# Kernel optimization log

Hardware: AMD Instinct MI355X
Metric: run time of the kernel (lower is better)

## Reference

```python
import jax, jax.numpy as jnp
import numpy as np

B, S, R, H = 16, 1024, 512, 512
HD = H // 2           # per-direction LSTM hidden
G = 4 * HD            # LSTM gate width
D_IN = 3 * H          # fusion encoder input size


def setup_inputs() -> dict:
    key = jax.random.key(0)
    ks = jax.random.split(key, 14)
    sc_ref = 1.0 / np.sqrt(H)
    sc_ih = 1.0 / np.sqrt(D_IN)
    sc_hh = 1.0 / np.sqrt(HD)
    return {
        "src_enc_state": jax.random.normal(ks[0], (2, B, HD), jnp.float32),  # unused by module
        "src_memory_bank": jax.random.normal(ks[1], (S, B, H), jnp.float32),
        "ref_memory_bank": jax.random.normal(ks[2], (R, B, H), jnp.float32),
        "W_ref": jax.random.normal(ks[3], (H, H), jnp.float32) * sc_ref,
        "b_ref": jax.random.normal(ks[4], (H,), jnp.float32) * sc_ref,
        "W_ih_f": jax.random.normal(ks[5], (G, D_IN), jnp.float32) * sc_ih,
        "W_hh_f": jax.random.normal(ks[6], (G, HD), jnp.float32) * sc_hh,
        "b_ih_f": jax.random.normal(ks[7], (G,), jnp.float32) * sc_hh,
        "b_hh_f": jax.random.normal(ks[8], (G,), jnp.float32) * sc_hh,
        "W_ih_b": jax.random.normal(ks[9], (G, D_IN), jnp.float32) * sc_ih,
        "W_hh_b": jax.random.normal(ks[10], (G, HD), jnp.float32) * sc_hh,
        "b_ih_b": jax.random.normal(ks[11], (G,), jnp.float32) * sc_hh,
        "b_hh_b": jax.random.normal(ks[12], (G,), jnp.float32) * sc_hh,
        "ref_length": jnp.full((B,), R, dtype=jnp.int32),  # full lengths -> pack is identity
    }


def _lstm_dir(x, W_ih, W_hh, b_ih, b_hh, reverse=False):
    """Single-direction LSTM (PyTorch gate order i,f,g,o). x: [T,B,D] -> [T,B,HD]."""
    if reverse:
        x = x[::-1]
    xg = jnp.einsum('tbd,gd->tbg', x, W_ih) + b_ih + b_hh  # precompute input gates

    def step(carry, xg_t):
        h, c = carry
        g = xg_t + h @ W_hh.T
        i, f, gg, o = jnp.split(g, 4, axis=-1)
        c = jax.nn.sigmoid(f) * c + jax.nn.sigmoid(i) * jnp.tanh(gg)
        h = jax.nn.sigmoid(o) * jnp.tanh(c)
        return (h, c), h

    h0 = jnp.zeros((x.shape[1], W_hh.shape[1]), x.dtype)
    _, hs = jax.lax.scan(step, (h0, h0), xg)
    return hs[::-1] if reverse else hs


def reference(src_enc_state, src_memory_bank, ref_memory_bank,
              W_ref, b_ref,
              W_ih_f, W_hh_f, b_ih_f, b_hh_f,
              W_ih_b, W_hh_b, b_ih_b, b_hh_b,
              ref_length):
    # --- co-attention ---
    # h_s = tanh(linear_ref(src)) : [B,S,H]
    h_s = jnp.tanh(jnp.einsum('sbh,oh->bso', src_memory_bank, W_ref) + b_ref)
    h_r = ref_memory_bank.transpose(1, 0, 2)                      # [B,R,H]
    l = jnp.einsum('bsh,brh->bsr', h_s, h_r)                      # scores [B,S,R]
    a_s = jax.nn.softmax(l, axis=1)                               # softmax over src dim
    a_r = jax.nn.softmax(l, axis=2)                               # softmax over ref dim
    c_s = jnp.einsum('brh,bsr->bhs', h_r, a_s)                    # [B,H,S]
    s_t = h_s.transpose(0, 2, 1)                                  # [B,H,S]
    cat_sc = jnp.concatenate([s_t, c_s], axis=1)                  # [B,2H,S]
    c_r = jnp.einsum('bks,bsr->brk', cat_sc, a_r)                 # [B,R,2H]
    bilstm_in = jnp.concatenate([c_r, h_r], axis=2).transpose(1, 0, 2)  # [R,B,3H]
    # --- fusion BiLSTM encoder (all lengths == R, so packing is identity) ---
    hf = _lstm_dir(bilstm_in, W_ih_f, W_hh_f, b_ih_f, b_hh_f, reverse=False)
    hb = _lstm_dir(bilstm_in, W_ih_b, W_hh_b, b_ih_b, b_hh_b, reverse=True)
    return jnp.concatenate([hf, hb], axis=-1)                     # [R,B,H]
```

## Files before the change

### kernel.cpp

```cpp
#include <hip/hip_runtime.h>
#include <hip/hip_bf16.h>
#include <math.h>

#define B_   16
#define S_   1024
#define R_   512
#define H_   512
#define HD_  256
#define G_   1024
#define DIN_ 1536

template<int EPI, int REMAP_A>
__global__ __launch_bounds__(256) void gemm_mk_nk(
    const float* __restrict__ A, long a_rs, long a_bs,
    const float* __restrict__ Bm, long b_rs, long b_bs,
    float* __restrict__ C, long c_rs, long c_bs,
    const float* __restrict__ bias,
    int M, int N, int K)
{
    __shared__ float As[16][68];
    __shared__ float Bs[16][68];
    const int bb = blockIdx.z;
    const float* Ab = A + (long)bb * a_bs;
    const float* Bb = Bm + (long)bb * b_bs;
    float* Cb = C + (long)bb * c_bs;
    const int m0 = blockIdx.y * 64, n0 = blockIdx.x * 64;
    const int tid = threadIdx.x;
    const int tx = tid & 15, ty = tid >> 4;
    const int lr = tid >> 2;
    const int lk = (tid & 3) << 2;

    long arow;
    {
        int m = m0 + lr;
        if (REMAP_A) arow = (long)((m % S_) * B_ + (m / S_)) * a_rs;
        else         arow = (long)m * a_rs;
    }
    const long brow = (long)(n0 + lr) * b_rs;

    float acc[4][4] = {};
    for (int k0 = 0; k0 < K; k0 += 16) {
        float4 av = *(const float4*)(Ab + arow + k0 + lk);
        float4 bv = *(const float4*)(Bb + brow + k0 + lk);
        As[lk + 0][lr] = av.x; As[lk + 1][lr] = av.y;
        As[lk + 2][lr] = av.z; As[lk + 3][lr] = av.w;
        Bs[lk + 0][lr] = bv.x; Bs[lk + 1][lr] = bv.y;
        Bs[lk + 2][lr] = bv.z; Bs[lk + 3][lr] = bv.w;
        __syncthreads();
#pragma unroll
        for (int kk = 0; kk < 16; ++kk) {
            float4 a = *(const float4*)&As[kk][ty << 2];
            float4 b = *(const float4*)&Bs[kk][tx << 2];
            acc[0][0] += a.x * b.x; acc[0][1] += a.x * b.y; acc[0][2] += a.x * b.z; acc[0][3] += a.x * b.w;
            acc[1][0] += a.y * b.x; acc[1][1] += a.y * b.y; acc[1][2] += a.y * b.z; acc[1][3] += a.y * b.w;
            acc[2][0] += a.z * b.x; acc[2][1] += a.z * b.y; acc[2][2] += a.z * b.z; acc[2][3] += a.z * b.w;
            acc[3][0] += a.w * b.x; acc[3][1] += a.w * b.y; acc[3][2] += a.w * b.z; acc[3][3] += a.w * b.w;
        }
        __syncthreads();
    }
#pragma unroll
    for (int i = 0; i < 4; ++i) {
        const int m = m0 + (ty << 2) + i;
#pragma unroll
        for (int j = 0; j < 4; ++j) {
            const int n = n0 + (tx << 2) + j;
            float v = acc[i][j];
            if (EPI == 1) v = tanhf(v + bias[n]);
            Cb[(long)m * c_rs + n] = v;
        }
    }
}

__device__ inline unsigned short bf16_rtn(float x)
{
    unsigned u = __float_as_uint(x);
    u += 0x7FFFu + ((u >> 16) & 1);
    return (unsigned short)(u >> 16);
}

__device__ inline unsigned pk_bf16(float lo, float hi)
{
    return (unsigned)bf16_rtn(lo) | ((unsigned)bf16_rtn(hi) << 16);
}

__global__ __launch_bounds__(256) void pack_bf16(const float* __restrict__ src,
                                                 unsigned short* __restrict__ dst,
                                                 long n4)
{
    const long i = (long)blockIdx.x * 256 + threadIdx.x;
    if (i >= n4) return;
    const float4 v = *((const float4*)src + i);
    uint2 u;
    u.x = pk_bf16(v.x, v.y);
    u.y = pk_bf16(v.z, v.w);
    *((uint2*)dst + i) = u;
}

__global__ __launch_bounds__(256) void softmax_rows(float* __restrict__ l)
{
    const int lane = threadIdx.x & 63;
    const int wv = threadIdx.x >> 6;
    const long row = (long)blockIdx.x * 4 + wv;
    float* p = l + row * R_;
    float4 v0 = ((const float4*)p)[lane * 2];
    float4 v1 = ((const float4*)p)[lane * 2 + 1];
    float m = fmaxf(fmaxf(fmaxf(v0.x, v0.y), fmaxf(v0.z, v0.w)),
                    fmaxf(fmaxf(v1.x, v1.y), fmaxf(v1.z, v1.w)));
#pragma unroll
    for (int o = 32; o; o >>= 1) m = fmaxf(m, __shfl_xor(m, o));
    v0.x = __expf(v0.x - m); v0.y = __expf(v0.y - m);
    v0.z = __expf(v0.z - m); v0.w = __expf(v0.w - m);
    v1.x = __expf(v1.x - m); v1.y = __expf(v1.y - m);
    v1.z = __expf(v1.z - m); v1.w = __expf(v1.w - m);
    float s = v0.x + v0.y + v0.z + v0.w + v1.x + v1.y + v1.z + v1.w;
#pragma unroll
    for (int o = 32; o; o >>= 1) s += __shfl_xor(s, o);
    const float inv = 1.f / s;
    v0.x *= inv; v0.y *= inv; v0.z *= inv; v0.w *= inv;
    v1.x *= inv; v1.y *= inv; v1.z *= inv; v1.w *= inv;
    ((float4*)p)[lane * 2] = v0;
    ((float4*)p)[lane * 2 + 1] = v1;
}

__global__ __launch_bounds__(512) void softmax_cols(const float* __restrict__ l,
                                                    unsigned short* __restrict__ asb)
{
    const int b = blockIdx.y;
    const int rl = threadIdx.x & 127;
    const int r = blockIdx.x * 128 + rl;
    const int sg = threadIdx.x >> 7;
    const int s0 = sg * (S_ / 4), s1 = s0 + S_ / 4;
    const float* base = l + (long)b * S_ * R_ + r;
    __shared__ float red[4][128];

    float pm = -1e30f;
    for (int s = s0; s < s1; ++s) pm = fmaxf(pm, base[(long)s * R_]);
    red[sg][rl] = pm;
    __syncthreads();
    const float m = fmaxf(fmaxf(red[0][rl], red[1][rl]), fmaxf(red[2][rl], red[3][rl]));
    __syncthreads();

    float ps = 0.f;
    for (int s = s0; s < s1; ++s) ps += __expf(base[(long)s * R_] - m);
    red[sg][rl] = ps;
    __syncthreads();
    const float inv = 1.f / (red[0][rl] + red[1][rl] + red[2][rl] + red[3][rl]);

    unsigned short* ob = asb + (long)b * S_ * R_ + r;
    for (int s = s0; s < s1; ++s)
        ob[(long)s * R_] = bf16_rtn(__expf(base[(long)s * R_] - m) * inv);
}

__global__ __launch_bounds__(256) void transpose_hs(const float* __restrict__ hs,
                                                    unsigned short* __restrict__ catb)
{
    __shared__ float tile[32][33];
    const int b = blockIdx.z;
    const int s0 = blockIdx.x * 32, h0 = blockIdx.y * 32;
    const int tx = threadIdx.x, ty = threadIdx.y;
#pragma unroll
    for (int i = 0; i < 32; i += 8)
        tile[ty + i][tx] = hs[((long)b * S_ + s0 + ty + i) * H_ + h0 + tx];
    __syncthreads();
#pragma unroll
    for (int i = 0; i < 32; i += 8)
        catb[((long)b * 2 * H_ + h0 + ty + i) * S_ + s0 + tx] = bf16_rtn(tile[tx][ty + i]);
}

__global__ __launch_bounds__(256) void transpose_ref(const float* __restrict__ ref,
                                                     unsigned short* __restrict__ refT)
{
    __shared__ float tile[32][33];
    const int b = blockIdx.z;
    const int r0 = blockIdx.x * 32, h0 = blockIdx.y * 32;
    const int tx = threadIdx.x, ty = threadIdx.y;
#pragma unroll
    for (int i = 0; i < 32; i += 8)
        tile[ty + i][tx] = ref[((long)(r0 + ty + i) * B_ + b) * H_ + h0 + tx];
    __syncthreads();
#pragma unroll
    for (int i = 0; i < 32; i += 8)
        refT[((long)b * H_ + h0 + ty + i) * R_ + r0 + tx] = bf16_rtn(tile[tx][ty + i]);
}

__global__ __launch_bounds__(256) void transpose_arT(const float* __restrict__ l,
                                                     unsigned short* __restrict__ arT)
{
    __shared__ float tile[32][33];
    const int b = blockIdx.z;
    const int s0 = blockIdx.x * 32, r0 = blockIdx.y * 32;
    const int tx = threadIdx.x, ty = threadIdx.y;
#pragma unroll
    for (int i = 0; i < 32; i += 8)
        tile[ty + i][tx] = l[((long)b * S_ + s0 + ty + i) * R_ + r0 + tx];
    __syncthreads();
#pragma unroll
    for (int i = 0; i < 32; i += 8)
        arT[((long)b * R_ + r0 + ty + i) * S_ + s0 + tx] = bf16_rtn(tile[tx][ty + i]);
}

__global__ __launch_bounds__(256) void build_bin(const float* __restrict__ cr,
                                                 const float* __restrict__ ref,
                                                 unsigned short* __restrict__ binb)
{
    const long idx4 = (long)blockIdx.x * blockDim.x + threadIdx.x;
    if (idx4 >= (long)R_ * B_ * DIN_ / 4) return;
    const long f = idx4 * 4;
    const int d = (int)(f % DIN_);
    const long tb = f / DIN_;
    const int b = (int)(tb % B_);
    const int t = (int)(tb / B_);
    float4 v;
    if (d < 2 * H_) v = *(const float4*)(cr + ((long)b * R_ + t) * (2 * H_) + d);
    else            v = *(const float4*)(ref + ((long)t * B_ + b) * H_ + (d - 2 * H_));
    uint2 u;
    u.x = pk_bf16(v.x, v.y);
    u.y = pk_bf16(v.z, v.w);
    *((uint2*)binb + idx4) = u;
}

__global__ __launch_bounds__(256) void transpose_w_bf16(
    const float* __restrict__ Whh_f, const float* __restrict__ Whh_b,
    unsigned* __restrict__ WB)
{
    const int g = blockIdx.x * 256 + threadIdx.x;
    const int q2 = blockIdx.y;
    const int dir = blockIdx.z;
    const float* W = dir ? Whh_b : Whh_f;
    const float4 a = *(const float4*)(W + (long)g * HD_ + q2 * 8);
    const float4 b = *(const float4*)(W + (long)g * HD_ + q2 * 8 + 4);
    uint4 u;
    u.x = pk_bf16(a.x, a.y);
    u.y = pk_bf16(a.z, a.w);
    u.z = pk_bf16(b.x, b.y);
    u.w = pk_bf16(b.z, b.w);
    *((uint4*)WB + ((long)dir * 32 + q2) * 1024 + g) = u;
}

typedef __attribute__((ext_vector_type(4))) float f32x4;
typedef __attribute__((ext_vector_type(8))) short bf16x8;

__device__ inline bf16x8 u4_to_b8(uint4 u)
{
    bf16x8 r;
    __builtin_memcpy(&r, &u, 16);
    return r;
}

template<int CT>
__global__ __launch_bounds__(256) void gemm56(
    const unsigned short* __restrict__ A, long a_bs, int lda,
    const unsigned short* __restrict__ Bm, long b_bs, int ldb,
    void* __restrict__ Cv, long c_bs, int ldc, int K)
{
    const int bb = blockIdx.z;
    const int n0 = blockIdx.x * 64, m0 = blockIdx.y * 64;
    const int lane = threadIdx.x & 63, w = threadIdx.x >> 6;
    const int lr = lane & 15, lk = lane >> 4;
    const unsigned short* ap = A + bb * a_bs + (long)(m0 + lr) * lda + lk * 8;
    const unsigned short* bp = Bm + bb * b_bs + (long)(n0 + 16 * w + lr) * ldb + lk * 8;

    f32x4 acc[4];
#pragma unroll
    for (int mi = 0; mi < 4; ++mi) acc[mi] = (f32x4){0.f, 0.f, 0.f, 0.f};

    for (int k0 = 0; k0 < K; k0 += 32) {
        const bf16x8 bfr = *(const bf16x8*)(bp + k0);
#pragma unroll
        for (int mi = 0; mi < 4; ++mi) {
            const bf16x8 afr = *(const bf16x8*)(ap + (long)mi * 16 * lda + k0);
            acc[mi] = __builtin_amdgcn_mfma_f32_16x16x32_bf16(afr, bfr, acc[mi], 0, 0, 0);
        }
    }
    const int n = n0 + 16 * w + lr;
    if (CT == 0) {
        unsigned short* C = (unsigned short*)Cv + bb * c_bs;
#pragma unroll
        for (int mi = 0; mi < 4; ++mi)
#pragma unroll
            for (int r = 0; r < 4; ++r)
                C[(long)(m0 + 16 * mi + lk * 4 + r) * ldc + n] = bf16_rtn(acc[mi][r]);
    } else {
        float* C = (float*)Cv + bb * c_bs;
#pragma unroll
        for (int mi = 0; mi < 4; ++mi) {
            float4 v = make_float4(acc[mi][0], acc[mi][1], acc[mi][2], acc[mi][3]);
            *(float4*)&C[(long)n * ldc + m0 + 16 * mi + lk * 4] = v;
        }
    }
}

__global__ __launch_bounds__(256) void gemm_xg_mfma(
    const unsigned short* __restrict__ binb, const unsigned short* __restrict__ Wb,
    const float* __restrict__ bihf, const float* __restrict__ bhhf,
    const float* __restrict__ bihb, const float* __restrict__ bhhb,
    float* __restrict__ xgf2, float* __restrict__ xgb2)
{
    const int dir = blockIdx.z;
    const int n0 = blockIdx.x * 64;
    const int m0 = blockIdx.y * 64;
    const int lane = threadIdx.x & 63, w = threadIdx.x >> 6;
    const int lr = lane & 15, lk = lane >> 4;
    const unsigned short* Wd = Wb + (long)dir * G_ * DIN_;
    const float* bi = dir ? bihb : bihf;
    const float* bh = dir ? bhhb : bhhf;
    float* xg = dir ? xgb2 : xgf2;

    const int n = n0 + 16 * w + lr;
    const unsigned short* bp = Wd + (long)n * DIN_ + lk * 8;
    const unsigned short* ap = binb + (long)(m0 + lr) * DIN_ + lk * 8;

    f32x4 acc[4];
#pragma unroll
    for (int mi = 0; mi < 4; ++mi) acc[mi] = (f32x4){0.f, 0.f, 0.f, 0.f};

    for (int k0 = 0; k0 < DIN_; k0 += 32) {
        const bf16x8 bfr = *(const bf16x8*)(bp + k0);
#pragma unroll
        for (int mi = 0; mi < 4; ++mi) {
            const bf16x8 afr = *(const bf16x8*)(ap + (long)mi * 16 * DIN_ + k0);
            acc[mi] = __builtin_amdgcn_mfma_f32_16x16x32_bf16(afr, bfr, acc[mi], 0, 0, 0);
        }
    }
    const float bias = bi[n] + bh[n];
#pragma unroll
    for (int mi = 0; mi < 4; ++mi)
#pragma unroll
        for (int r = 0; r < 4; ++r) {
            const int m = m0 + 16 * mi + lk * 4 + r;
            xg[(long)m * G_ + n] = acc[mi][r] + bias;
        }
}

#define NBD 4

__device__ inline float sig_(float x) { return 1.f / (1.f + __expf(-x)); }
__device__ inline float tanh_(float x) {
    float ax = fabsf(x);
    float t = 1.f - 2.f / (1.f + __expf(2.f * ax));
    return copysignf(t, x);
}

__global__ __launch_bounds__(256) void lstm_scan_s(
    const float* __restrict__ xg_f, const float* __restrict__ xg_b,
    const uint4* __restrict__ WBu, unsigned short* __restrict__ hbuf,
    unsigned* __restrict__ flags, float* __restrict__ out)
{
    const int blk = blockIdx.x;
    const int dir = blk >> 2;
    const int j = blk & 3;
    const float* xg = dir ? xg_b : xg_f;
    const uint4* Wg = WBu + (long)dir * 32768;
    unsigned short* hb = hbuf + dir * (2 * B_ * HD_);
    unsigned* fl = flags + dir * 64;

    __shared__ uint4 WL[32 * 256];
    __shared__ unsigned short h_lds[16 * 264];

    const int tid = threadIdx.x;
    const int lane = tid & 63, w = tid >> 6;
    const int lcol = lane & 15, lkg = lane >> 4;

    for (int idx = tid; idx < 32 * 256; idx += 256) {
        const int q2 = idx >> 8, loc = idx & 255;
        const int g = loc >> 6, c = loc & 63;
        WL[idx] = Wg[q2 * 1024 + g * 256 + 64 * j + c];
    }
    float c_reg[4] = {};
    const int col = 64 * j + 16 * w + lcol;
    __syncthreads();

    for (int t = 0; t < R_; ++t) {
        const int tt = dir ? (R_ - 1 - t) : t;
        const int p = t & 1;

        float xgv[4][4];
#pragma unroll
        for (int g = 0; g < 4; ++g)
#pragma unroll
            for (int r = 0; r < 4; ++r)
                xgv[g][r] = xg[((long)tt * B_ + lkg * 4 + r) * G_ + g * 256 + col];

        if (t > 0) {
            if (tid < 64) {
                while (true) {
                    unsigned v = (lane < NBD)
                        ? __hip_atomic_load(&fl[lane * 16], __ATOMIC_RELAXED,
                                            __HIP_MEMORY_SCOPE_AGENT)
                        : 0xFFFFFFFFu;
                    if (__all(v >= (unsigned)t)) break;
                    __builtin_amdgcn_s_sleep(1);
                }
            }
            __syncthreads();
            __builtin_amdgcn_fence(__ATOMIC_ACQUIRE, "agent");
        }

        for (int i = tid; i < 512; i += 256) {
            const int b = i >> 5, c8 = (i & 31) * 8;
            *(uint4*)&h_lds[b * 264 + c8] =
                *(const uint4*)&hb[p * (B_ * HD_) + b * HD_ + c8];
        }
        __syncthreads();

        f32x4 acc[4];
#pragma unroll
        for (int g = 0; g < 4; ++g) acc[g] = (f32x4){0.f, 0.f, 0.f, 0.f};
        const unsigned short* hrow = &h_lds[lcol * 264 + lkg * 8];
#pragma unroll
        for (int kk = 0; kk < 8; ++kk) {
            const bf16x8 a_ = *(const bf16x8*)(hrow + 32 * kk);
#pragma unroll
            for (int g = 0; g < 4; ++g) {
                const uint4 wv = WL[(4 * kk + lkg) * 256 + g * 64 + 16 * w + lcol];
                acc[g] = __builtin_amdgcn_mfma_f32_16x16x32_bf16(
                    a_, u4_to_b8(wv), acc[g], 0, 0, 0);
            }
        }

#pragma unroll
        for (int r = 0; r < 4; ++r) {
            const int batch = lkg * 4 + r;
            const float iv = acc[0][r] + xgv[0][r];
            const float fv = acc[1][r] + xgv[1][r];
            const float gv = acc[2][r] + xgv[2][r];
            const float ov = acc[3][r] + xgv[3][r];
            float c = sig_(fv) * c_reg[r] + sig_(iv) * tanh_(gv);
            c_reg[r] = c;
            const float h = sig_(ov) * tanh_(c);
            out[((long)tt * B_ + batch) * (2 * HD_) + dir * HD_ + col] = h;
            hb[(p ^ 1) * (B_ * HD_) + batch * HD_ + col] = bf16_rtn(h);
        }
        __syncthreads();
        if (tid == 0) {
            __threadfence();
            __hip_atomic_store(&fl[j * 16], (unsigned)(t + 1), __ATOMIC_RELAXED,
                               __HIP_MEMORY_SCOPE_AGENT);
        }
    }
}

extern "C" void kernel_launch(void* const* d_in, const int* in_sizes, int n_in,
                              void* d_out, int out_size, void* d_ws, size_t ws_size,
                              hipStream_t stream)
{
    const float* src  = (const float*)d_in[1];
    const float* ref  = (const float*)d_in[2];
    const float* Wref = (const float*)d_in[3];
    const float* bref = (const float*)d_in[4];
    const float* Wihf = (const float*)d_in[5];
    const float* Whhf = (const float*)d_in[6];
    const float* bihf = (const float*)d_in[7];
    const float* bhhf = (const float*)d_in[8];
    const float* Wihb = (const float*)d_in[9];
    const float* Whhb = (const float*)d_in[10];
    const float* bihb = (const float*)d_in[11];
    const float* bhhb = (const float*)d_in[12];
    float* out = (float*)d_out;

    float* ws = (float*)d_ws;
    float* hs   = ws + 0L;
    float* l    = ws + 8388608L;
    unsigned short* as_bf = (unsigned short*)(ws + 16777216L);
    unsigned short* refT  = (unsigned short*)(ws + 20971520L);
    unsigned short* a_rT  = (unsigned short*)(ws + 23068672L);
    unsigned short* catb  = (unsigned short*)(ws + 27262976L);
    unsigned short* binb  = (unsigned short*)(ws + 35651584L);
    unsigned* WB = (unsigned*)(ws + 41943040L);
    unsigned short* Wib = (unsigned short*)(ws + 42205184L);
    unsigned short* hbuf = (unsigned short*)(ws + 43778048L);
    unsigned* flags = (unsigned*)(ws + 43786240L);
    float* cr  = hs;
    float* xgf = l;
    float* xgb = ws + 16777216L;

    hipMemsetAsync(hbuf, 0, 2 * 2 * B_ * HD_ * 2 + 512, stream);

    transpose_w_bf16<<<dim3(4, 32, 2), 256, 0, stream>>>(Whhf, Whhb, WB);
    pack_bf16<<<dim3((G_ * DIN_ / 4 + 255) / 256), 256, 0, stream>>>(
        Wihf, Wib, (long)G_ * DIN_ / 4);
    pack_bf16<<<dim3((G_ * DIN_ / 4 + 255) / 256), 256, 0, stream>>>(
        Wihb, Wib + (long)G_ * DIN_, (long)G_ * DIN_ / 4);

    gemm_mk_nk<1, 1><<<dim3(8, 256, 1), 256, 0, stream>>>(
        src, H_, 0, Wref, H_, 0, hs, H_, 0, bref, B_ * S_, H_, H_);

    gemm_mk_nk<0, 0><<<dim3(8, 16, B_), 256, 0, stream>>>(
        hs, H_, (long)S_ * H_, ref, (long)B_ * H_, H_, l, R_, (long)S_ * R_,
        nullptr, S_, R_, H_);

    softmax_cols<<<dim3(R_ / 128, B_), 512, 0, stream>>>(l, as_bf);
    softmax_rows<<<(B_ * S_) / 4, 256, 0, stream>>>(l);

    transpose_ref<<<dim3(R_ / 32, H_ / 32, B_), dim3(32, 8), 0, stream>>>(ref, refT);
    transpose_arT<<<dim3(S_ / 32, R_ / 32, B_), dim3(32, 8), 0, stream>>>(l, a_rT);

    transpose_hs<<<dim3(S_ / 32, H_ / 32, B_), dim3(32, 8), 0, stream>>>(hs, catb);

    gemm56<0><<<dim3(S_ / 64, H_ / 64, B_), 256, 0, stream>>>(
        refT, (long)H_ * R_, R_, as_bf, (long)S_ * R_, R_,
        (void*)(catb + (long)H_ * S_), (long)2 * H_ * S_, S_, R_);

    gemm56<1><<<dim3(R_ / 64, 2 * H_ / 64, B_), 256, 0, stream>>>(
        catb, (long)2 * H_ * S_, S_, a_rT, (long)R_ * S_, S_,
        (void*)cr, (long)R_ * 2 * H_, 2 * H_, S_);

    build_bin<<<(R_ * B_ * DIN_ / 4 + 255) / 256, 256, 0, stream>>>(cr, ref, binb);

    gemm_xg_mfma<<<dim3(G_ / 64, R_ * B_ / 64, 2), 256, 0, stream>>>(
        binb, Wib, bihf, bhhf, bihb, bhhb, xgf, xgb);

    lstm_scan_s<<<dim3(2 * NBD), dim3(256), 0, stream>>>(
        xgf, xgb, (const uint4*)WB, hbuf, flags, out);
}
```

Baseline: 2.864 ms.

## Replace fp32 SIMT GEMMs with split-bf16 MFMA GEMMs and cache LSTM h in LDS

The two fp32 SIMT GEMMs (the tanh(src·W_ref) projection and the score GEMM) become MFMA GEMMs. Each operand is split into a bf16 hi and lo part and three MFMA products are accumulated, which keeps close to fp32 accuracy. This needs extra pack passes over src, ref, W_ref and hs, which add memory traffic. Separately, the LSTM scan double-buffers h in LDS: each block writes its own h slice locally and copies only the other three blocks' slices from global memory, and the output store moves after the flag release to shorten the serial critical path.

```diff
diff --git a/kernel.cpp b/kernel.cpp
--- a/kernel.cpp
+++ b/kernel.cpp
@@ -10,67 +10,6 @@
 #define G_   1024
 #define DIN_ 1536
 
-template<int EPI, int REMAP_A>
-__global__ __launch_bounds__(256) void gemm_mk_nk(
-    const float* __restrict__ A, long a_rs, long a_bs,
-    const float* __restrict__ Bm, long b_rs, long b_bs,
-    float* __restrict__ C, long c_rs, long c_bs,
-    const float* __restrict__ bias,
-    int M, int N, int K)
-{
-    __shared__ float As[16][68];
-    __shared__ float Bs[16][68];
-    const int bb = blockIdx.z;
-    const float* Ab = A + (long)bb * a_bs;
-    const float* Bb = Bm + (long)bb * b_bs;
-    float* Cb = C + (long)bb * c_bs;
-    const int m0 = blockIdx.y * 64, n0 = blockIdx.x * 64;
-    const int tid = threadIdx.x;
-    const int tx = tid & 15, ty = tid >> 4;
-    const int lr = tid >> 2;
-    const int lk = (tid & 3) << 2;
-
-    long arow;
-    {
-        int m = m0 + lr;
-        if (REMAP_A) arow = (long)((m % S_) * B_ + (m / S_)) * a_rs;
-        else         arow = (long)m * a_rs;
-    }
-    const long brow = (long)(n0 + lr) * b_rs;
-
-    float acc[4][4] = {};
-    for (int k0 = 0; k0 < K; k0 += 16) {
-        float4 av = *(const float4*)(Ab + arow + k0 + lk);
-        float4 bv = *(const float4*)(Bb + brow + k0 + lk);
-        As[lk + 0][lr] = av.x; As[lk + 1][lr] = av.y;
-        As[lk + 2][lr] = av.z; As[lk + 3][lr] = av.w;
-        Bs[lk + 0][lr] = bv.x; Bs[lk + 1][lr] = bv.y;
-        Bs[lk + 2][lr] = bv.z; Bs[lk + 3][lr] = bv.w;
-        __syncthreads();
-#pragma unroll
-        for (int kk = 0; kk < 16; ++kk) {
-            float4 a = *(const float4*)&As[kk][ty << 2];
-            float4 b = *(const float4*)&Bs[kk][tx << 2];
-            acc[0][0] += a.x * b.x; acc[0][1] += a.x * b.y; acc[0][2] += a.x * b.z; acc[0][3] += a.x * b.w;
-            acc[1][0] += a.y * b.x; acc[1][1] += a.y * b.y; acc[1][2] += a.y * b.z; acc[1][3] += a.y * b.w;
-            acc[2][0] += a.z * b.x; acc[2][1] += a.z * b.y; acc[2][2] += a.z * b.z; acc[2][3] += a.z * b.w;
-            acc[3][0] += a.w * b.x; acc[3][1] += a.w * b.y; acc[3][2] += a.w * b.z; acc[3][3] += a.w * b.w;
-        }
-        __syncthreads();
-    }
-#pragma unroll
-    for (int i = 0; i < 4; ++i) {
-        const int m = m0 + (ty << 2) + i;
-#pragma unroll
-        for (int j = 0; j < 4; ++j) {
-            const int n = n0 + (tx << 2) + j;
-            float v = acc[i][j];
-            if (EPI == 1) v = tanhf(v + bias[n]);
-            Cb[(long)m * c_rs + n] = v;
-        }
-    }
-}
-
 __device__ inline unsigned short bf16_rtn(float x)
 {
     unsigned u = __float_as_uint(x);
@@ -94,6 +33,86 @@
     u.x = pk_bf16(v.x, v.y);
     u.y = pk_bf16(v.z, v.w);
     *((uint2*)dst + i) = u;
+}
+
+__global__ __launch_bounds__(256) void pack_hilo(const float* __restrict__ src,
+                                                 unsigned short* __restrict__ hi,
+                                                 unsigned short* __restrict__ lo,
+                                                 long n4)
+{
+    const long i = (long)blockIdx.x * 256 + threadIdx.x;
+    if (i >= n4) return;
+    const float4 v = *((const float4*)src + i);
+    float vv[4] = {v.x, v.y, v.z, v.w};
+    unsigned short h[4], L[4];
+#pragma unroll
+    for (int e = 0; e < 4; ++e) {
+        h[e] = bf16_rtn(vv[e]);
+        const float hf = __uint_as_float((unsigned)h[e] << 16);
+        L[e] = bf16_rtn(vv[e] - hf);
+    }
+    uint2 uh, ul;
+    uh.x = (unsigned)h[0] | ((unsigned)h[1] << 16);
+    uh.y = (unsigned)h[2] | ((unsigned)h[3] << 16);
+    ul.x = (unsigned)L[0] | ((unsigned)L[1] << 16);
+    ul.y = (unsigned)L[2] | ((unsigned)L[3] << 16);
+    *((uint2*)hi + i) = uh;
+    *((uint2*)lo + i) = ul;
+}
+
+typedef __attribute__((ext_vector_type(4))) float f32x4;
+typedef __attribute__((ext_vector_type(8))) short bf16x8;
+
+__device__ inline bf16x8 u4_to_b8(uint4 u)
+{
+    bf16x8 r;
+    __builtin_memcpy(&r, &u, 16);
+    return r;
+}
+
+__global__ __launch_bounds__(256) void gemm_split(
+    const unsigned short* __restrict__ Ahi, const unsigned short* __restrict__ Alo,
+    long a_bs, long lda,
+    const unsigned short* __restrict__ Bhi, const unsigned short* __restrict__ Blo,
+    long b_bs, long ldb,
+    float* __restrict__ C, long c_bs, int ldc,
+    const float* __restrict__ bias, int do_tanh, int K)
+{
+    const int bb = blockIdx.z;
+    const int n0 = blockIdx.x * 64, m0 = blockIdx.y * 64;
+    const int lane = threadIdx.x & 63, w = threadIdx.x >> 6;
+    const int lr = lane & 15, lk = lane >> 4;
+    const long boff = bb * b_bs + (long)(n0 + 16 * w + lr) * ldb + lk * 8;
+    const unsigned short* bh = Bhi + boff;
+    const unsigned short* bl = Blo + boff;
+
+    f32x4 acc[4];
+#pragma unroll
+    for (int mi = 0; mi < 4; ++mi) acc[mi] = (f32x4){0.f, 0.f, 0.f, 0.f};
+
+    for (int k0 = 0; k0 < K; k0 += 32) {
+        const bf16x8 bhf = *(const bf16x8*)(bh + k0);
+        const bf16x8 blf = *(const bf16x8*)(bl + k0);
+#pragma unroll
+        for (int mi = 0; mi < 4; ++mi) {
+            const long aoff = bb * a_bs + (long)(m0 + 16 * mi + lr) * lda + lk * 8 + k0;
+            const bf16x8 ahf = *(const bf16x8*)(Ahi + aoff);
+            const bf16x8 alf = *(const bf16x8*)(Alo + aoff);
+            acc[mi] = __builtin_amdgcn_mfma_f32_16x16x32_bf16(ahf, bhf, acc[mi], 0, 0, 0);
+            acc[mi] = __builtin_amdgcn_mfma_f32_16x16x32_bf16(alf, bhf, acc[mi], 0, 0, 0);
+            acc[mi] = __builtin_amdgcn_mfma_f32_16x16x32_bf16(ahf, blf, acc[mi], 0, 0, 0);
+        }
+    }
+    const int n = n0 + 16 * w + lr;
+    const float bv = bias ? bias[n] : 0.f;
+#pragma unroll
+    for (int mi = 0; mi < 4; ++mi)
+#pragma unroll
+        for (int r = 0; r < 4; ++r) {
+            float v = acc[mi][r] + bv;
+            if (do_tanh) v = tanhf(v);
+            C[bb * c_bs + (long)(m0 + 16 * mi + lk * 4 + r) * ldc + n] = v;
+        }
 }
 
 __global__ __launch_bounds__(256) void softmax_rows(float* __restrict__ l)
@@ -237,16 +256,6 @@
     *((uint4*)WB + ((long)dir * 32 + q2) * 1024 + g) = u;
 }
 
-typedef __attribute__((ext_vector_type(4))) float f32x4;
-typedef __attribute__((ext_vector_type(8))) short bf16x8;
-
-__device__ inline bf16x8 u4_to_b8(uint4 u)
-{
-    bf16x8 r;
-    __builtin_memcpy(&r, &u, 16);
-    return r;
-}
-
 template<int CT>
 __global__ __launch_bounds__(256) void gemm56(
     const unsigned short* __restrict__ A, long a_bs, int lda,
@@ -335,11 +344,6 @@
 #define NBD 4
 
 __device__ inline float sig_(float x) { return 1.f / (1.f + __expf(-x)); }
-__device__ inline float tanh_(float x) {
-    float ax = fabsf(x);
-    float t = 1.f - 2.f / (1.f + __expf(2.f * ax));
-    return copysignf(t, x);
-}
 
 __global__ __launch_bounds__(256) void lstm_scan_s(
     const float* __restrict__ xg_f, const float* __restrict__ xg_b,
@@ -355,7 +359,7 @@
     unsigned* fl = flags + dir * 64;
 
     __shared__ uint4 WL[32 * 256];
-    __shared__ unsigned short h_lds[16 * 264];
+    __shared__ unsigned short h_lds[2][16 * 264];
 
     const int tid = threadIdx.x;
     const int lane = tid & 63, w = tid >> 6;
@@ -366,6 +370,7 @@
         const int g = loc >> 6, c = loc & 63;
         WL[idx] = Wg[q2 * 1024 + g * 256 + 64 * j + c];
     }
+    for (int i = tid; i < 16 * 264; i += 256) h_lds[0][i] = 0;
     float c_reg[4] = {};
     const int col = 64 * j + 16 * w + lcol;
     __syncthreads();
@@ -394,19 +399,22 @@
             }
             __syncthreads();
             __builtin_amdgcn_fence(__ATOMIC_ACQUIRE, "agent");
-        }
-
-        for (int i = tid; i < 512; i += 256) {
-            const int b = i >> 5, c8 = (i & 31) * 8;
-            *(uint4*)&h_lds[b * 264 + c8] =
-                *(const uint4*)&hb[p * (B_ * HD_) + b * HD_ + c8];
-        }
-        __syncthreads();
+
+            for (int i = tid; i < 384; i += 256) {
+                const int si = i >> 7;
+                const int jo = si + (si >= j);
+                const int rr = i & 127;
+                const int b = rr >> 3, c8 = 64 * jo + (rr & 7) * 8;
+                *(uint4*)&h_lds[p][b * 264 + c8] =
+                    *(const uint4*)&hb[p * (B_ * HD_) + b * HD_ + c8];
+            }
+            __syncthreads();
+        }
 
         f32x4 acc[4];
 #pragma unroll
         for (int g = 0; g < 4; ++g) acc[g] = (f32x4){0.f, 0.f, 0.f, 0.f};
-        const unsigned short* hrow = &h_lds[lcol * 264 + lkg * 8];
+        const unsigned short* hrow = &h_lds[p][lcol * 264 + lkg * 8];
 #pragma unroll
         for (int kk = 0; kk < 8; ++kk) {
             const bf16x8 a_ = *(const bf16x8*)(hrow + 32 * kk);
@@ -418,6 +426,7 @@
             }
         }
 
+        float hsv[4];
 #pragma unroll
         for (int r = 0; r < 4; ++r) {
             const int batch = lkg * 4 + r;
@@ -425,11 +434,17 @@
             const float fv = acc[1][r] + xgv[1][r];
             const float gv = acc[2][r] + xgv[2][r];
             const float ov = acc[3][r] + xgv[3][r];
-            float c = sig_(fv) * c_reg[r] + sig_(iv) * tanh_(gv);
+            float ax = fabsf(gv);
+            float tg = copysignf(1.f - 2.f / (1.f + __expf(2.f * ax)), gv);
+            float c = sig_(fv) * c_reg[r] + sig_(iv) * tg;
             c_reg[r] = c;
-            const float h = sig_(ov) * tanh_(c);
-            out[((long)tt * B_ + batch) * (2 * HD_) + dir * HD_ + col] = h;
-            hb[(p ^ 1) * (B_ * HD_) + batch * HD_ + col] = bf16_rtn(h);
+            float ac = fabsf(c);
+            float tc = copysignf(1.f - 2.f / (1.f + __expf(2.f * ac)), c);
+            const float h = sig_(ov) * tc;
+            hsv[r] = h;
+            const unsigned short hb16 = bf16_rtn(h);
+            hb[(p ^ 1) * (B_ * HD_) + batch * HD_ + col] = hb16;
+            h_lds[p ^ 1][batch * 264 + col] = hb16;
         }
         __syncthreads();
         if (tid == 0) {
@@ -437,6 +452,9 @@
             __hip_atomic_store(&fl[j * 16], (unsigned)(t + 1), __ATOMIC_RELAXED,
                                __HIP_MEMORY_SCOPE_AGENT);
         }
+#pragma unroll
+        for (int r = 0; r < 4; ++r)
+            out[((long)tt * B_ + lkg * 4 + r) * (2 * HD_) + dir * HD_ + col] = hsv[r];
     }
 }
 
@@ -470,6 +488,14 @@
     unsigned short* Wib = (unsigned short*)(ws + 42205184L);
     unsigned short* hbuf = (unsigned short*)(ws + 43778048L);
     unsigned* flags = (unsigned*)(ws + 43786240L);
+    unsigned short* srchi = (unsigned short*)(ws + 27262976L);
+    unsigned short* srclo = (unsigned short*)(ws + 31457280L);
+    unsigned short* refhi = (unsigned short*)(ws + 35651584L);
+    unsigned short* reflo = (unsigned short*)(ws + 37748736L);
+    unsigned short* hshi  = (unsigned short*)(ws + 16777216L);
+    unsigned short* hslo  = (unsigned short*)(ws + 20971520L);
+    unsigned short* wrefhi = (unsigned short*)(ws + 43786368L);
+    unsigned short* wreflo = (unsigned short*)(ws + 44048512L);
     float* cr  = hs;
     float* xgf = l;
     float* xgb = ws + 16777216L;
@@ -481,13 +507,20 @@
         Wihf, Wib, (long)G_ * DIN_ / 4);
     pack_bf16<<<dim3((G_ * DIN_ / 4 + 255) / 256), 256, 0, stream>>>(
         Wihb, Wib + (long)G_ * DIN_, (long)G_ * DIN_ / 4);
-
-    gemm_mk_nk<1, 1><<<dim3(8, 256, 1), 256, 0, stream>>>(
-        src, H_, 0, Wref, H_, 0, hs, H_, 0, bref, B_ * S_, H_, H_);
-
-    gemm_mk_nk<0, 0><<<dim3(8, 16, B_), 256, 0, stream>>>(
-        hs, H_, (long)S_ * H_, ref, (long)B_ * H_, H_, l, R_, (long)S_ * R_,
-        nullptr, S_, R_, H_);
+    pack_hilo<<<dim3(8192), 256, 0, stream>>>(src, srchi, srclo, (long)S_ * B_ * H_ / 4);
+    pack_hilo<<<dim3(4096), 256, 0, stream>>>(ref, refhi, reflo, (long)R_ * B_ * H_ / 4);
+    pack_hilo<<<dim3(256), 256, 0, stream>>>(Wref, wrefhi, wreflo, (long)H_ * H_ / 4);
+
+    gemm_split<<<dim3(H_ / 64, S_ / 64, B_), 256, 0, stream>>>(
+        srchi, srclo, H_, (long)B_ * H_,
+        wrefhi, wreflo, 0, H_,
+        hs, (long)S_ * H_, H_, bref, 1, H_);
+
+    pack_hilo<<<dim3(8192), 256, 0, stream>>>(hs, hshi, hslo, (long)B_ * S_ * H_ / 4);
+    gemm_split<<<dim3(R_ / 64, S_ / 64, B_), 256, 0, stream>>>(
+        hshi, hslo, (long)S_ * H_, H_,
+        refhi, reflo, H_, (long)B_ * H_,
+        l, (long)S_ * R_, R_, nullptr, 0, H_);
 
     softmax_cols<<<dim3(R_ / 128, B_), 512, 0, stream>>>(l, as_bf);
     softmax_rows<<<(B_ * S_) / 4, 256, 0, stream>>>(l);
```

After: 2.943 ms. 2.7% more time.

## Keep own h slice in LDS and exchange peers' hidden state via atomic loads

Applied to the files above, without the earlier changes.

The LSTM scan now double-buffers the hidden state in LDS. Each block writes its own slice locally and fetches only the three peer blocks' slices from global memory, using relaxed agent-scope atomic loads and packed 32-bit stores. This removes the explicit threadfence before the flag store, the acquire fence after polling, and one full reload of h per step. The output store is moved after the flag release so it stays off the critical path. The risk is the memory ordering: the flag store is relaxed and has no fence, so it relies on the ordering of agent-scope atomics.

```diff
diff --git a/kernel.cpp b/kernel.cpp
--- a/kernel.cpp
+++ b/kernel.cpp
@@ -335,15 +335,10 @@
 #define NBD 4
 
 __device__ inline float sig_(float x) { return 1.f / (1.f + __expf(-x)); }
-__device__ inline float tanh_(float x) {
-    float ax = fabsf(x);
-    float t = 1.f - 2.f / (1.f + __expf(2.f * ax));
-    return copysignf(t, x);
-}
 
 __global__ __launch_bounds__(256) void lstm_scan_s(
     const float* __restrict__ xg_f, const float* __restrict__ xg_b,
-    const uint4* __restrict__ WBu, unsigned short* __restrict__ hbuf,
+    const uint4* __restrict__ WBu, unsigned* __restrict__ hbu32,
     unsigned* __restrict__ flags, float* __restrict__ out)
 {
     const int blk = blockIdx.x;
@@ -351,11 +346,11 @@
     const int j = blk & 3;
     const float* xg = dir ? xg_b : xg_f;
     const uint4* Wg = WBu + (long)dir * 32768;
-    unsigned short* hb = hbuf + dir * (2 * B_ * HD_);
+    unsigned* hbu = hbu32 + dir * 4096;
     unsigned* fl = flags + dir * 64;
 
     __shared__ uint4 WL[32 * 256];
-    __shared__ unsigned short h_lds[16 * 264];
+    __shared__ unsigned short h_lds[2][16 * 264];
 
     const int tid = threadIdx.x;
     const int lane = tid & 63, w = tid >> 6;
@@ -366,6 +361,7 @@
         const int g = loc >> 6, c = loc & 63;
         WL[idx] = Wg[q2 * 1024 + g * 256 + 64 * j + c];
     }
+    for (int i = tid; i < 16 * 264; i += 256) h_lds[0][i] = 0;
     float c_reg[4] = {};
     const int col = 64 * j + 16 * w + lcol;
     __syncthreads();
@@ -393,20 +389,24 @@
                 }
             }
             __syncthreads();
-            __builtin_amdgcn_fence(__ATOMIC_ACQUIRE, "agent");
-        }
-
-        for (int i = tid; i < 512; i += 256) {
-            const int b = i >> 5, c8 = (i & 31) * 8;
-            *(uint4*)&h_lds[b * 264 + c8] =
-                *(const uint4*)&hb[p * (B_ * HD_) + b * HD_ + c8];
-        }
-        __syncthreads();
+
+            for (int i = tid; i < 1536; i += 256) {
+                const int b = i / 96, k = i - (i / 96) * 96;
+                const int sl = k >> 5;
+                const int jo = sl + (sl >= j);
+                const int ku = 32 * jo + (k & 31);
+                const unsigned v = __hip_atomic_load(
+                    &hbu[p * 2048 + b * 128 + ku],
+                    __ATOMIC_RELAXED, __HIP_MEMORY_SCOPE_AGENT);
+                *(unsigned*)&h_lds[p][b * 264 + 2 * ku] = v;
+            }
+            __syncthreads();
+        }
 
         f32x4 acc[4];
 #pragma unroll
         for (int g = 0; g < 4; ++g) acc[g] = (f32x4){0.f, 0.f, 0.f, 0.f};
-        const unsigned short* hrow = &h_lds[lcol * 264 + lkg * 8];
+        const unsigned short* hrow = &h_lds[p][lcol * 264 + lkg * 8];
 #pragma unroll
         for (int kk = 0; kk < 8; ++kk) {
             const bf16x8 a_ = *(const bf16x8*)(hrow + 32 * kk);
@@ -418,6 +418,7 @@
             }
         }
 
+        float hsv[4];
 #pragma unroll
         for (int r = 0; r < 4; ++r) {
             const int batch = lkg * 4 + r;
@@ -425,18 +426,30 @@
             const float fv = acc[1][r] + xgv[1][r];
             const float gv = acc[2][r] + xgv[2][r];
             const float ov = acc[3][r] + xgv[3][r];
-            float c = sig_(fv) * c_reg[r] + sig_(iv) * tanh_(gv);
+            float ax = fabsf(gv);
+            float tg = copysignf(1.f - 2.f / (1.f + __expf(2.f * ax)), gv);
+            float c = sig_(fv) * c_reg[r] + sig_(iv) * tg;
             c_reg[r] = c;
-            const float h = sig_(ov) * tanh_(c);
-            out[((long)tt * B_ + batch) * (2 * HD_) + dir * HD_ + col] = h;
-            hb[(p ^ 1) * (B_ * HD_) + batch * HD_ + col] = bf16_rtn(h);
+            float ac = fabsf(c);
+            float tc = copysignf(1.f - 2.f / (1.f + __expf(2.f * ac)), c);
+            const float h = sig_(ov) * tc;
+            hsv[r] = h;
+            const unsigned short hb16 = bf16_rtn(h);
+            h_lds[p ^ 1][batch * 264 + col] = hb16;
+            const unsigned nb = (unsigned)__shfl_xor((int)(unsigned)hb16, 1);
+            if ((lcol & 1) == 0) {
+                const unsigned pkd = (unsigned)hb16 | (nb << 16);
+                __hip_atomic_store(&hbu[(p ^ 1) * 2048 + batch * 128 + (col >> 1)],
+                                   pkd, __ATOMIC_RELAXED, __HIP_MEMORY_SCOPE_AGENT);
+            }
         }
         __syncthreads();
-        if (tid == 0) {
-            __threadfence();
+        if (tid == 0)
             __hip_atomic_store(&fl[j * 16], (unsigned)(t + 1), __ATOMIC_RELAXED,
                                __HIP_MEMORY_SCOPE_AGENT);
-        }
+#pragma unroll
+        for (int r = 0; r < 4; ++r)
+            out[((long)tt * B_ + lkg * 4 + r) * (2 * HD_) + dir * HD_ + col] = hsv[r];
     }
 }
 
@@ -468,13 +481,13 @@
     unsigned short* binb  = (unsigned short*)(ws + 35651584L);
     unsigned* WB = (unsigned*)(ws + 41943040L);
     unsigned short* Wib = (unsigned short*)(ws + 42205184L);
-    unsigned short* hbuf = (unsigned short*)(ws + 43778048L);
+    unsigned* hbu32 = (unsigned*)(ws + 43778048L);
     unsigned* flags = (unsigned*)(ws + 43786240L);
     float* cr  = hs;
     float* xgf = l;
     float* xgb = ws + 16777216L;
 
-    hipMemsetAsync(hbuf, 0, 2 * 2 * B_ * HD_ * 2 + 512, stream);
+    hipMemsetAsync(hbu32, 0, 2 * 2 * B_ * HD_ * 2 + 512, stream);
 
     transpose_w_bf16<<<dim3(4, 32, 2), 256, 0, stream>>>(Whhf, Whhb, WB);
     pack_bf16<<<dim3((G_ * DIN_ / 4 + 255) / 256), 256, 0, stream>>>(
@@ -511,5 +524,5 @@
         binb, Wib, bihf, bhhf, bihb, bhhb, xgf, xgb);
 
     lstm_scan_s<<<dim3(2 * NBD), dim3(256), 0, stream>>>(
-        xgf, xgb, (const uint4*)WB, hbuf, flags, out);
-}
+        xgf, xgb, (const uint4*)WB, hbu32, flags, out);
+}
```

Result: slower. 3.253 ms (+13.6%).
